# Kernel tuning notes

Measured on AMD Instinct MI355X. Metric: run time of the kernel, lower is better.

The kernel has to match this reference:

```python
import jax, jax.numpy as jnp
import numpy as np

JACCARD_THRESH = 0.5
NEGPOS_RATIO = 3
V0, V1 = 0.1, 0.2  # SSD encoding variances


def setup_inputs() -> dict:
    key = jax.random.key(0)
    k1, k2, k3, k4, k5, k6, k7 = jax.random.split(key, 7)
    B, P, C, O = 128, 8732, 21, 16
    loc_data = jax.random.normal(k1, (B, P, 4), dtype=jnp.float32)
    conf_data = jax.random.normal(k2, (B, P, C), dtype=jnp.float32)
    # default boxes in center form (cx, cy, w, h), all in [0,1]
    cxcy = jax.random.uniform(k3, (P, 2), minval=0.05, maxval=0.95)
    wh = jax.random.uniform(k4, (P, 2), minval=0.05, maxval=0.6)
    dbox_list = jnp.concatenate([cxcy, wh], axis=1).astype(jnp.float32)
    # ground-truth boxes in corner form with guaranteed positive extent
    tl = jax.random.uniform(k5, (B, O, 2), minval=0.0, maxval=0.6)
    sz = jax.random.uniform(k6, (B, O, 2), minval=0.05, maxval=0.35)
    labels = jax.random.randint(k7, (B, O, 1), 0, C - 1).astype(jnp.float32)
    targets = jnp.concatenate([tl, tl + sz, labels], axis=2)
    return {"loc_data": loc_data, "conf_data": conf_data,
            "dbox_list": dbox_list, "targets": targets}


def _match_one(truths, labels, dbox):
    """SSD match for one image. truths:[O,4] corner, labels:[O], dbox:[P,4] center."""
    pf = jnp.concatenate([dbox[:, :2] - dbox[:, 2:] * 0.5,
                          dbox[:, :2] + dbox[:, 2:] * 0.5], axis=1)  # point form [P,4]
    lt = jnp.maximum(truths[:, None, :2], pf[None, :, :2])
    rb = jnp.minimum(truths[:, None, 2:], pf[None, :, 2:])
    whi = jnp.clip(rb - lt, 0.0)
    inter = whi[..., 0] * whi[..., 1]                                # [O,P]
    area_t = (truths[:, 2] - truths[:, 0]) * (truths[:, 3] - truths[:, 1])
    area_p = dbox[:, 2] * dbox[:, 3]
    ov = inter / (area_t[:, None] + area_p[None, :] - inter)         # jaccard [O,P]
    best_prior_idx = jnp.argmax(ov, axis=1)                          # [O]
    bto = jnp.max(ov, axis=0)                                        # [P]
    bti = jnp.argmax(ov, axis=0)                                     # [P]
    bto = bto.at[best_prior_idx].set(2.0)
    O = truths.shape[0]
    bti = jax.lax.fori_loop(0, O, lambda j, b: b.at[best_prior_idx[j]].set(j), bti)
    matched = truths[bti]                                            # [P,4]
    conf = labels[bti].astype(jnp.int32) + 1
    conf = jnp.where(bto < JACCARD_THRESH, 0, conf)
    g_cxcy = ((matched[:, :2] + matched[:, 2:]) * 0.5 - dbox[:, :2]) / (V0 * dbox[:, 2:])
    g_wh = jnp.log((matched[:, 2:] - matched[:, :2]) / dbox[:, 2:]) / V1
    return jnp.concatenate([g_cxcy, g_wh], axis=1), conf


def reference(loc_data, conf_data, dbox_list, targets):
    B, P, C = conf_data.shape
    loc_t, conf_t = jax.vmap(_match_one, in_axes=(0, 0, None))(
        targets[..., :4], targets[..., 4], dbox_list)
    pos = conf_t > 0                                                  # [B,P]
    # smooth L1 (beta=1), summed over positives
    ad = jnp.abs(loc_data - loc_t)
    sl1 = jnp.where(ad < 1.0, 0.5 * ad * ad, ad - 0.5)
    loss_l = jnp.sum(jnp.where(pos[..., None], sl1, 0.0))
    # per-prior cross entropy
    logp = jax.nn.log_softmax(conf_data, axis=-1)
    ce = -jnp.take_along_axis(logp, conf_t[..., None], axis=-1)[..., 0]  # [B,P]
    # hard negative mining via double argsort (rank in descending order)
    ce_neg = jnp.where(pos, 0.0, ce)
    loss_idx = jnp.argsort(-ce_neg, axis=1)
    idx_rank = jnp.argsort(loss_idx, axis=1)
    num_pos = jnp.sum(pos, axis=1, keepdims=True)
    num_neg = jnp.minimum(num_pos * NEGPOS_RATIO, P)
    neg = idx_rank < num_neg
    sel = pos | neg
    loss_c = jnp.sum(jnp.where(sel, ce, 0.0))
    N = jnp.sum(num_pos).astype(loc_data.dtype)
    return jnp.stack([loss_l / N, loss_c / N])
```

## Files before the change

kernel.cpp:

```cpp
#include <hip/hip_runtime.h>
#include <cstddef>
#include <cstdint>

#define Bn 128
#define Pn 8732
#define Cn 21
#define On 16
#define MAGIC 0x13579BDFu

__device__ __forceinline__ void argmax_combine(float& v, int& p, float v2, int p2) {
  if (v2 > v || (v2 == v && p2 < p)) { v = v2; p = p2; }
}

__device__ __forceinline__ void cp16_lds(const float4* g, float4* l) {
  __builtin_amdgcn_global_load_lds(
      (const __attribute__((address_space(1))) unsigned int*)g,
      (__attribute__((address_space(3))) unsigned int*)l, 16, 0, 0);
}

__global__ __launch_bounds__(1024) void fused_kernel(
    const float* __restrict__ loc, const float* __restrict__ conf,
    const float* __restrict__ dbox, const float* __restrict__ targets,
    unsigned int* __restrict__ res, float* __restrict__ out) {
  const int b = blockIdx.x;
  const int tid = threadIdx.x;
  const int wv = tid >> 6, lane = tid & 63;

  __shared__ float s_ce[Pn];
  __shared__ float s_stage[16][1344];
  __shared__ unsigned char s_bti[Pn];
  __shared__ unsigned hist[16][256];
  __shared__ float s_tt[80];
  __shared__ float s_ar[On];
  __shared__ float s_mv[On][16];
  __shared__ int   s_mp[On][16];
  __shared__ int   s_bp[On];
  __shared__ float s_redf[2][16];
  __shared__ int   s_redi[16];
  __shared__ int   s_sfx[256];
  __shared__ int   s_wsum[4];
  __shared__ unsigned s_prefix;
  __shared__ int s_kk, s_np;

  const size_t confBase = (size_t)b * Pn * Cn;

  {
    const float4* src = (const float4*)(conf + confBase + (size_t)wv * (64 * Cn));
    float4* dst = (float4*)s_stage[wv];
    #pragma unroll
    for (int q = 0; q < 6; q++)
      if (lane + 64 * q < 336) cp16_lds(src + lane + 64 * q, dst + 64 * q);
  }

  if (tid < 80) s_tt[tid] = targets[b * 80 + tid];
  __syncthreads();
  if (tid < On)
    s_ar[tid] = (s_tt[tid*5+2] - s_tt[tid*5+0]) * (s_tt[tid*5+3] - s_tt[tid*5+1]);
  __syncthreads();

  {
    float bestv[On]; int bestp[On];
    #pragma unroll
    for (int j = 0; j < On; j++) { bestv[j] = -1.0f; bestp[j] = 0x7fffffff; }

    for (int p = tid; p < Pn; p += 1024) {
      float4 d = ((const float4*)dbox)[p];
      float px1 = d.x - d.z * 0.5f, py1 = d.y - d.w * 0.5f;
      float px2 = d.x + d.z * 0.5f, py2 = d.y + d.w * 0.5f;
      float ap = d.z * d.w;
      float mv = -1.0f; int mj = 0;
      #pragma unroll
      for (int j = 0; j < On; j++) {
        float lx = fmaxf(s_tt[j*5+0], px1);
        float ly = fmaxf(s_tt[j*5+1], py1);
        float rx = fminf(s_tt[j*5+2], px2);
        float ry = fminf(s_tt[j*5+3], py2);
        float w = fmaxf(rx - lx, 0.0f), h = fmaxf(ry - ly, 0.0f);
        float inter = w * h;
        float ov = inter / (s_ar[j] + ap - inter);
        if (ov > bestv[j]) { bestv[j] = ov; bestp[j] = p; }
        if (ov > mv) { mv = ov; mj = j; }
      }
      s_bti[p] = (unsigned char)(mj | ((mv >= 0.5f) ? 16 : 0));
    }

    #pragma unroll
    for (int j = 0; j < On; j++) {
      float v = bestv[j]; int p = bestp[j];
      #pragma unroll
      for (int off = 32; off; off >>= 1) {
        float v2 = __shfl_down(v, off);
        int p2 = __shfl_down(p, off);
        argmax_combine(v, p, v2, p2);
      }
      if (lane == 0) { s_mv[j][wv] = v; s_mp[j][wv] = p; }
    }
  }

  for (int ci = wv; ci < 137; ci += 16) {
    asm volatile("s_waitcnt vmcnt(0)" ::: "memory");
    const int rows = (ci == 136) ? 28 : 64;
    if (lane < rows) {
      const int p = ci * 64 + lane;
      const float* x = s_stage[wv] + lane * Cn;
      float m = x[0];
      #pragma unroll
      for (int q = 1; q < Cn; q++) m = fmaxf(m, x[q]);
      float s = 0.0f;
      #pragma unroll
      for (int q = 0; q < Cn; q++) s += expf(x[q] - m);
      float lse = m + logf(s);
      s_ce[p] = lse - x[0];
    }
    asm volatile("s_waitcnt lgkmcnt(0)" ::: "memory");
    const int cn = ci + 16;
    if (cn < 137) {
      const int n4 = (cn == 136) ? 147 : 336;
      const float4* src = (const float4*)(conf + confBase + (size_t)cn * (64 * Cn));
      float4* dst = (float4*)s_stage[wv];
      #pragma unroll
      for (int q = 0; q < 6; q++)
        if (lane + 64 * q < n4) cp16_lds(src + lane + 64 * q, dst + 64 * q);
    }
  }
  __syncthreads();

  if (tid < On) {
    float v = s_mv[tid][0]; int p = s_mp[tid][0];
    #pragma unroll
    for (int w = 1; w < 16; w++) argmax_combine(v, p, s_mv[tid][w], s_mp[tid][w]);
    s_bp[tid] = p;
  }
  __syncthreads();
  if (tid == 0) {
    #pragma unroll
    for (int j = 0; j < On; j++)
      s_bti[s_bp[j]] = (unsigned char)(j | 16);
  }
  __syncthreads();

  float ce_r[9];
  float my_loc = 0.0f, my_cep = 0.0f; int my_np = 0;
  #pragma unroll
  for (int s9 = 0; s9 < 9; s9++) {
    ce_r[s9] = 0.0f;
    const int p = tid + 1024 * s9;
    if (p < Pn) {
      int pk = s_bti[p];
      float c0 = s_ce[p];
      int pos = pk >> 4, bt = pk & 15;
      ce_r[s9] = pos ? 0.0f : c0;
      if (pos) {
        my_np++;
        const float* t = &s_tt[bt * 5];
        int c = (int)t[4] + 1;
        const float* row = conf + confBase + (size_t)p * Cn;
        my_cep += c0 + row[0] - row[c];
        float4 d = ((const float4*)dbox)[p];
        float mx1 = t[0], my1 = t[1], mx2 = t[2], my2 = t[3];
        float g0 = ((mx1 + mx2) * 0.5f - d.x) / (0.1f * d.z);
        float g1 = ((my1 + my2) * 0.5f - d.y) / (0.1f * d.w);
        float g2 = logf((mx2 - mx1) / d.z) / 0.2f;
        float g3 = logf((my2 - my1) / d.w) / 0.2f;
        float4 ld = ((const float4*)loc)[(size_t)b * Pn + p];
        float g[4] = {g0, g1, g2, g3};
        float l[4] = {ld.x, ld.y, ld.z, ld.w};
        #pragma unroll
        for (int q = 0; q < 4; q++) {
          float ad = fabsf(l[q] - g[q]);
          my_loc += (ad < 1.0f) ? 0.5f * ad * ad : ad - 0.5f;
        }
      }
    }
  }
  {
    int np = my_np;
    #pragma unroll
    for (int off = 32; off; off >>= 1) np += __shfl_down(np, off);
    if (lane == 0) s_redi[wv] = np;
  }
  __syncthreads();
  if (tid == 0) {
    int np = 0;
    #pragma unroll
    for (int w = 0; w < 16; w++) np += s_redi[w];
    s_np = np;
  }
  __syncthreads();

  const int k = min(s_np * 3, Pn);
  int kk = max(k, 1);
  unsigned prefix = 0, maskb = 0;
  for (int shift = 24; shift >= 0; shift -= 8) {
    #pragma unroll
    for (int j = 0; j < 4; j++) hist[wv][lane * 4 + j] = 0;
    __syncthreads();
    #pragma unroll
    for (int s9 = 0; s9 < 9; s9++) {
      const int p = tid + 1024 * s9;
      if (p < Pn) {
        unsigned u = __float_as_uint(ce_r[s9]);
        if ((u & maskb) == prefix) atomicAdd(&hist[wv][(u >> shift) & 255u], 1u);
      }
    }
    __syncthreads();
    int v = 0;
    if (tid < 256) {
      int h = 0;
      #pragma unroll
      for (int w = 0; w < 16; w++) h += (int)hist[w][tid];
      v = h;
      #pragma unroll
      for (int off = 1; off < 64; off <<= 1) {
        int u2 = __shfl_down(v, off);
        if (lane + off < 64) v += u2;
      }
      if (lane == 0) s_wsum[tid >> 6] = v;
    }
    __syncthreads();
    if (tid < 256) {
      int S = v;
      #pragma unroll
      for (int w = 0; w < 4; w++) if (w > (tid >> 6)) S += s_wsum[w];
      s_sfx[tid] = S;
    }
    __syncthreads();
    if (tid < 256) {
      int S = s_sfx[tid];
      int Snext = (tid == 255) ? 0 : s_sfx[tid + 1];
      if (S >= kk && Snext < kk) {
        s_prefix = prefix | ((unsigned)tid << shift);
        s_kk = kk - Snext;
      }
    }
    __syncthreads();
    prefix = s_prefix; kk = s_kk;
    maskb |= 255u << shift;
    __syncthreads();
  }
  const float T = __uint_as_float(prefix);

  float sum_gt = 0.0f; int cnt_gt = 0;
  #pragma unroll
  for (int s9 = 0; s9 < 9; s9++) {
    const int p = tid + 1024 * s9;
    if (p < Pn) {
      float x = ce_r[s9];
      if (x > T) { sum_gt += x; cnt_gt++; }
    }
  }
  #pragma unroll
  for (int off = 32; off; off >>= 1) {
    sum_gt += __shfl_down(sum_gt, off);
    cnt_gt += __shfl_down(cnt_gt, off);
    my_loc += __shfl_down(my_loc, off);
    my_cep += __shfl_down(my_cep, off);
  }
  if (lane == 0) {
    s_redf[0][wv] = my_loc;
    s_redf[1][wv] = sum_gt + my_cep;
    s_redi[wv] = cnt_gt;
  }
  __syncthreads();
  if (tid == 0) {
    float ll = 0.0f, lc = 0.0f; int cg = 0;
    #pragma unroll
    for (int w = 0; w < 16; w++) {
      ll += s_redf[0][w]; lc += s_redf[1][w]; cg += s_redi[w];
    }
    if (k > 0) lc += (float)(k - cg) * T;
    atomicExch(&res[b * 4 + 0], __float_as_uint(ll));
    atomicExch(&res[b * 4 + 1], __float_as_uint(lc));
    atomicExch(&res[b * 4 + 2], (unsigned)s_np);
    __threadfence();
    atomicExch(&res[b * 4 + 3], MAGIC);
  }

  if (b == 0 && tid < 64) {
    float ll = 0.0f, lc = 0.0f; int np = 0;
    #pragma unroll
    for (int h = 0; h < 2; h++) {
      const int i = tid + 64 * h;
      while (atomicAdd(&res[i * 4 + 3], 0u) != MAGIC) { __builtin_amdgcn_s_sleep(8); }
      ll += __uint_as_float(atomicAdd(&res[i * 4 + 0], 0u));
      lc += __uint_as_float(atomicAdd(&res[i * 4 + 1], 0u));
      np += (int)atomicAdd(&res[i * 4 + 2], 0u);
    }
    #pragma unroll
    for (int off = 32; off; off >>= 1) {
      ll += __shfl_down(ll, off);
      lc += __shfl_down(lc, off);
      np += __shfl_down(np, off);
    }
    if (tid == 0) {
      float fN = (float)np;
      out[0] = ll / fN;
      out[1] = lc / fN;
    }
  }
}

extern "C" void kernel_launch(void* const* d_in, const int* in_sizes, int n_in,
                              void* d_out, int out_size, void* d_ws, size_t ws_size,
                              hipStream_t stream) {
  const float* loc_data  = (const float*)d_in[0];
  const float* conf_data = (const float*)d_in[1];
  const float* dbox      = (const float*)d_in[2];
  const float* targets   = (const float*)d_in[3];
  float* out = (float*)d_out;
  unsigned int* res = (unsigned int*)d_ws;

  fused_kernel<<<Bn, 1024, 0, stream>>>(loc_data, conf_data, dbox, targets, res, out);
}
```

Before: 234.9 us.

## Split each image across two 512-thread blocks with global-atomic cross-block exchange

Each image is now handled by two blocks of 512 threads instead of one 1024-thread block, so 256 blocks run instead of 128 and more CUs stream the confidence data. The two halves exchange their partial results through global memory using atomics and spin-waits: per-truth best-prior keys (via a 64-bit atomicMax), positive counts, per-pass radix-select histograms, and final partial sums. The histogram buffer now aliases the staging buffer in shared memory to cut LDS use. The cost is extra spin-wait synchronisation per radix pass, and correctness now rests on both blocks of a pair being resident at once. Workspace keys and flags are never cleared, so stale values from a previous call may be read as current ones.

```diff
diff --git a/kernel.cpp b/kernel.cpp
--- a/kernel.cpp
+++ b/kernel.cpp
@@ -6,6 +6,8 @@
 #define Pn 8732
 #define Cn 21
 #define On 16
+#define H0CNT 4352
+#define H1CNT 4380
 #define MAGIC 0x13579BDFu
 
 __device__ __forceinline__ void argmax_combine(float& v, int& p, float v2, int p2) {
@@ -18,34 +20,45 @@
       (__attribute__((address_space(3))) unsigned int*)l, 16, 0, 0);
 }
 
-__global__ __launch_bounds__(1024) void fused_kernel(
+__global__ __launch_bounds__(512, 4) void fused_kernel(
     const float* __restrict__ loc, const float* __restrict__ conf,
     const float* __restrict__ dbox, const float* __restrict__ targets,
-    unsigned int* __restrict__ res, float* __restrict__ out) {
-  const int b = blockIdx.x;
+    unsigned long long* __restrict__ keys,
+    unsigned int* __restrict__ adone,
+    unsigned int* __restrict__ nppost,
+    unsigned int* __restrict__ hpost,
+    unsigned int* __restrict__ fin,
+    unsigned int* __restrict__ res,
+    float* __restrict__ out) {
+  const int h = blockIdx.x & 1;
+  const int b = blockIdx.x >> 1;
   const int tid = threadIdx.x;
   const int wv = tid >> 6, lane = tid & 63;
-
-  __shared__ float s_ce[Pn];
-  __shared__ float s_stage[16][1344];
-  __shared__ unsigned char s_bti[Pn];
-  __shared__ unsigned hist[16][256];
+  const int halfBase = h ? H0CNT : 0;
+  const int halfCnt  = h ? H1CNT : H0CNT;
+  const int nChunks  = h ? 69 : 68;
+
+  __shared__ float s_stage[8][1344];
+  __shared__ float s_ce[H1CNT];
+  __shared__ unsigned char s_bti[H1CNT];
   __shared__ float s_tt[80];
   __shared__ float s_ar[On];
-  __shared__ float s_mv[On][16];
-  __shared__ int   s_mp[On][16];
+  __shared__ float s_mv[On][8];
+  __shared__ int   s_mp[On][8];
   __shared__ int   s_bp[On];
-  __shared__ float s_redf[2][16];
-  __shared__ int   s_redi[16];
+  __shared__ float s_redf[2][8];
+  __shared__ int   s_redi[8];
   __shared__ int   s_sfx[256];
   __shared__ int   s_wsum[4];
   __shared__ unsigned s_prefix;
   __shared__ int s_kk, s_np;
 
+  unsigned (*hist)[256] = (unsigned (*)[256])s_stage;
+
   const size_t confBase = (size_t)b * Pn * Cn;
 
   {
-    const float4* src = (const float4*)(conf + confBase + (size_t)wv * (64 * Cn));
+    const float4* src = (const float4*)(conf + confBase + (size_t)(halfBase + wv * 64) * Cn);
     float4* dst = (float4*)s_stage[wv];
     #pragma unroll
     for (int q = 0; q < 6; q++)
@@ -63,7 +76,8 @@
     #pragma unroll
     for (int j = 0; j < On; j++) { bestv[j] = -1.0f; bestp[j] = 0x7fffffff; }
 
-    for (int p = tid; p < Pn; p += 1024) {
+    for (int lp = tid; lp < halfCnt; lp += 512) {
+      const int p = halfBase + lp;
       float4 d = ((const float4*)dbox)[p];
       float px1 = d.x - d.z * 0.5f, py1 = d.y - d.w * 0.5f;
       float px2 = d.x + d.z * 0.5f, py2 = d.y + d.w * 0.5f;
@@ -75,15 +89,14 @@
         float ly = fmaxf(s_tt[j*5+1], py1);
         float rx = fminf(s_tt[j*5+2], px2);
         float ry = fminf(s_tt[j*5+3], py2);
-        float w = fmaxf(rx - lx, 0.0f), h = fmaxf(ry - ly, 0.0f);
-        float inter = w * h;
+        float w = fmaxf(rx - lx, 0.0f), hh = fmaxf(ry - ly, 0.0f);
+        float inter = w * hh;
         float ov = inter / (s_ar[j] + ap - inter);
         if (ov > bestv[j]) { bestv[j] = ov; bestp[j] = p; }
         if (ov > mv) { mv = ov; mj = j; }
       }
-      s_bti[p] = (unsigned char)(mj | ((mv >= 0.5f) ? 16 : 0));
-    }
-
+      s_bti[lp] = (unsigned char)(mj | ((mv >= 0.5f) ? 16 : 0));
+    }
     #pragma unroll
     for (int j = 0; j < On; j++) {
       float v = bestv[j]; int p = bestp[j];
@@ -96,12 +109,25 @@
       if (lane == 0) { s_mv[j][wv] = v; s_mp[j][wv] = p; }
     }
   }
-
-  for (int ci = wv; ci < 137; ci += 16) {
+  __syncthreads();
+  if (tid < On) {
+    float v = s_mv[tid][0]; int p = s_mp[tid][0];
+    #pragma unroll
+    for (int w = 1; w < 8; w++) argmax_combine(v, p, s_mv[tid][w], s_mp[tid][w]);
+    unsigned long long key =
+        (((unsigned long long)(__float_as_uint(v) | 0xC0000000u)) << 32)
+        | (unsigned long long)(0xFFFFFFFFu - (unsigned)p);
+    atomicMax(&keys[b * On + tid], key);
+  }
+  __threadfence();
+  __syncthreads();
+  if (tid == 0) atomicExch(&adone[b * 2 + h], MAGIC);
+
+  for (int ci = wv; ci < nChunks; ci += 8) {
     asm volatile("s_waitcnt vmcnt(0)" ::: "memory");
-    const int rows = (ci == 136) ? 28 : 64;
+    const int rows = (h && ci == 68) ? 28 : 64;
     if (lane < rows) {
-      const int p = ci * 64 + lane;
+      const int lp = ci * 64 + lane;
       const float* x = s_stage[wv] + lane * Cn;
       float m = x[0];
       #pragma unroll
@@ -109,14 +135,14 @@
       float s = 0.0f;
       #pragma unroll
       for (int q = 0; q < Cn; q++) s += expf(x[q] - m);
-      float lse = m + logf(s);
-      s_ce[p] = lse - x[0];
+      s_ce[lp] = m + logf(s) - x[0];
     }
     asm volatile("s_waitcnt lgkmcnt(0)" ::: "memory");
-    const int cn = ci + 16;
-    if (cn < 137) {
-      const int n4 = (cn == 136) ? 147 : 336;
-      const float4* src = (const float4*)(conf + confBase + (size_t)cn * (64 * Cn));
+    const int cn = ci + 8;
+    if (cn < nChunks) {
+      const int n4 = (h && cn == 68) ? 147 : 336;
+      const float4* src =
+          (const float4*)(conf + confBase + (size_t)(halfBase + cn * 64) * Cn);
       float4* dst = (float4*)s_stage[wv];
       #pragma unroll
       for (int q = 0; q < 6; q++)
@@ -125,17 +151,23 @@
   }
   __syncthreads();
 
+  if (tid == 0) {
+    while (atomicAdd(&adone[b * 2 + (1 - h)], 0u) != MAGIC)
+      __builtin_amdgcn_s_sleep(2);
+  }
+  __syncthreads();
   if (tid < On) {
-    float v = s_mv[tid][0]; int p = s_mp[tid][0];
-    #pragma unroll
-    for (int w = 1; w < 16; w++) argmax_combine(v, p, s_mv[tid][w], s_mp[tid][w]);
-    s_bp[tid] = p;
+    unsigned long long k64 = atomicAdd(&keys[b * On + tid], 0ull);
+    s_bp[tid] = (int)(0xFFFFFFFFu - (unsigned)(k64 & 0xFFFFFFFFull));
   }
   __syncthreads();
   if (tid == 0) {
     #pragma unroll
-    for (int j = 0; j < On; j++)
-      s_bti[s_bp[j]] = (unsigned char)(j | 16);
+    for (int j = 0; j < On; j++) {
+      int p = s_bp[j];
+      if (p >= halfBase && p < halfBase + halfCnt)
+        s_bti[p - halfBase] = (unsigned char)(j | 16);
+    }
   }
   __syncthreads();
 
@@ -144,14 +176,15 @@
   #pragma unroll
   for (int s9 = 0; s9 < 9; s9++) {
     ce_r[s9] = 0.0f;
-    const int p = tid + 1024 * s9;
-    if (p < Pn) {
-      int pk = s_bti[p];
-      float c0 = s_ce[p];
+    const int lp = tid + 512 * s9;
+    if (lp < halfCnt) {
+      int pk = s_bti[lp];
+      float c0 = s_ce[lp];
       int pos = pk >> 4, bt = pk & 15;
       ce_r[s9] = pos ? 0.0f : c0;
       if (pos) {
         my_np++;
+        const int p = halfBase + lp;
         const float* t = &s_tt[bt * 5];
         int c = (int)t[4] + 1;
         const float* row = conf + confBase + (size_t)p * Cn;
@@ -183,22 +216,28 @@
   if (tid == 0) {
     int np = 0;
     #pragma unroll
-    for (int w = 0; w < 16; w++) np += s_redi[w];
-    s_np = np;
+    for (int w = 0; w < 8; w++) np += s_redi[w];
+    atomicExch(&nppost[b * 2 + h], 0x5A5A0000u | (unsigned)np);
+    unsigned v;
+    while (((v = atomicAdd(&nppost[b * 2 + (1 - h)], 0u)) >> 16) != 0x5A5Au)
+      __builtin_amdgcn_s_sleep(2);
+    s_np = np + (int)(v & 0xFFFFu);
   }
   __syncthreads();
 
   const int k = min(s_np * 3, Pn);
   int kk = max(k, 1);
   unsigned prefix = 0, maskb = 0;
-  for (int shift = 24; shift >= 0; shift -= 8) {
+  #pragma unroll
+  for (int s = 0; s < 4; s++) {
+    const int shift = 24 - 8 * s;
     #pragma unroll
     for (int j = 0; j < 4; j++) hist[wv][lane * 4 + j] = 0;
     __syncthreads();
     #pragma unroll
     for (int s9 = 0; s9 < 9; s9++) {
-      const int p = tid + 1024 * s9;
-      if (p < Pn) {
+      const int lp = tid + 512 * s9;
+      if (lp < halfCnt) {
         unsigned u = __float_as_uint(ce_r[s9]);
         if ((u & maskb) == prefix) atomicAdd(&hist[wv][(u >> shift) & 255u], 1u);
       }
@@ -206,10 +245,16 @@
     __syncthreads();
     int v = 0;
     if (tid < 256) {
-      int h = 0;
-      #pragma unroll
-      for (int w = 0; w < 16; w++) h += (int)hist[w][tid];
-      v = h;
+      unsigned hown = 0;
+      #pragma unroll
+      for (int w = 0; w < 8; w++) hown += hist[w][tid];
+      const unsigned tag = (0x5B00u + s) << 16;
+      atomicExch(&hpost[(((size_t)b * 4 + s) * 2 + h) * 256 + tid], tag | hown);
+      unsigned pv;
+      unsigned int* pslot = &hpost[(((size_t)b * 4 + s) * 2 + (1 - h)) * 256 + tid];
+      while (((pv = atomicAdd(pslot, 0u)) & 0xFFFF0000u) != tag)
+        __builtin_amdgcn_s_sleep(2);
+      v = (int)(hown + (pv & 0xFFFFu));
       #pragma unroll
       for (int off = 1; off < 64; off <<= 1) {
         int u2 = __shfl_down(v, off);
@@ -243,8 +288,8 @@
   float sum_gt = 0.0f; int cnt_gt = 0;
   #pragma unroll
   for (int s9 = 0; s9 < 9; s9++) {
-    const int p = tid + 1024 * s9;
-    if (p < Pn) {
+    const int lp = tid + 512 * s9;
+    if (lp < halfCnt) {
       float x = ce_r[s9];
       if (x > T) { sum_gt += x; cnt_gt++; }
     }
@@ -262,26 +307,39 @@
     s_redi[wv] = cnt_gt;
   }
   __syncthreads();
+
   if (tid == 0) {
-    float ll = 0.0f, lc = 0.0f; int cg = 0;
-    #pragma unroll
-    for (int w = 0; w < 16; w++) {
-      ll += s_redf[0][w]; lc += s_redf[1][w]; cg += s_redi[w];
-    }
-    if (k > 0) lc += (float)(k - cg) * T;
-    atomicExch(&res[b * 4 + 0], __float_as_uint(ll));
-    atomicExch(&res[b * 4 + 1], __float_as_uint(lc));
-    atomicExch(&res[b * 4 + 2], (unsigned)s_np);
-    __threadfence();
-    atomicExch(&res[b * 4 + 3], MAGIC);
-  }
-
-  if (b == 0 && tid < 64) {
+    float loc_o = 0.0f, cg_o = 0.0f; int cnt_o = 0;
+    #pragma unroll
+    for (int w = 0; w < 8; w++) {
+      loc_o += s_redf[0][w]; cg_o += s_redf[1][w]; cnt_o += s_redi[w];
+    }
+    if (h == 1) {
+      atomicExch(&fin[b * 4 + 0], __float_as_uint(loc_o));
+      atomicExch(&fin[b * 4 + 1], __float_as_uint(cg_o));
+      atomicExch(&fin[b * 4 + 2], (unsigned)cnt_o);
+      __threadfence();
+      atomicExch(&fin[b * 4 + 3], MAGIC);
+    } else {
+      while (atomicAdd(&fin[b * 4 + 3], 0u) != MAGIC) __builtin_amdgcn_s_sleep(2);
+      float ll = loc_o + __uint_as_float(atomicAdd(&fin[b * 4 + 0], 0u));
+      float lc = cg_o + __uint_as_float(atomicAdd(&fin[b * 4 + 1], 0u));
+      int cg = cnt_o + (int)atomicAdd(&fin[b * 4 + 2], 0u);
+      if (k > 0) lc += (float)(k - cg) * T;
+      atomicExch(&res[b * 4 + 0], __float_as_uint(ll));
+      atomicExch(&res[b * 4 + 1], __float_as_uint(lc));
+      atomicExch(&res[b * 4 + 2], (unsigned)s_np);
+      __threadfence();
+      atomicExch(&res[b * 4 + 3], MAGIC);
+    }
+  }
+
+  if (blockIdx.x == 0 && tid < 64) {
     float ll = 0.0f, lc = 0.0f; int np = 0;
     #pragma unroll
-    for (int h = 0; h < 2; h++) {
-      const int i = tid + 64 * h;
-      while (atomicAdd(&res[i * 4 + 3], 0u) != MAGIC) { __builtin_amdgcn_s_sleep(8); }
+    for (int g = 0; g < 2; g++) {
+      const int i = tid + 64 * g;
+      while (atomicAdd(&res[i * 4 + 3], 0u) != MAGIC) __builtin_amdgcn_s_sleep(8);
       ll += __uint_as_float(atomicAdd(&res[i * 4 + 0], 0u));
       lc += __uint_as_float(atomicAdd(&res[i * 4 + 1], 0u));
       np += (int)atomicAdd(&res[i * 4 + 2], 0u);
@@ -308,7 +366,15 @@
   const float* dbox      = (const float*)d_in[2];
   const float* targets   = (const float*)d_in[3];
   float* out = (float*)d_out;
-  unsigned int* res = (unsigned int*)d_ws;
-
-  fused_kernel<<<Bn, 1024, 0, stream>>>(loc_data, conf_data, dbox, targets, res, out);
+
+  char* ws = (char*)d_ws;
+  unsigned long long* keys = (unsigned long long*)ws;
+  unsigned int* adone  = (unsigned int*)(ws + 16384);
+  unsigned int* nppost = (unsigned int*)(ws + 16384 + 1024);
+  unsigned int* fin    = (unsigned int*)(ws + 16384 + 2048);
+  unsigned int* res    = (unsigned int*)(ws + 16384 + 4096);
+  unsigned int* hpost  = (unsigned int*)(ws + 16384 + 8192);
+
+  fused_kernel<<<2 * Bn, 512, 0, stream>>>(loc_data, conf_data, dbox, targets,
+                                           keys, adone, nppost, hpost, fin, res, out);
 }
```

New measurement: 256.3 us. 1.09x slower.
